# Kernel optimization log

Measured on AMD Instinct MI355X. Metric: run time of the kernel, lower is better.

## Reference

```python
import jax, jax.numpy as jnp
import numpy as np

B, NA, C, NG = 32, 32768, 81, 24
POS_IOU, NEG_IOU, NPR = 0.5, 0.4, 3
VXY, VWH = 0.1, 0.2
NEG_BIG = 1e30


def cxcywh_to_xyxy(b):
    xy, wh = b[..., :2], b[..., 2:]
    return jnp.concatenate([xy - 0.5 * wh, xy + 0.5 * wh], axis=-1)


def box_iou_xyxy(a, g):
    # a: [Na,4], g: [Ng,4] -> [Na,Ng]
    lt = jnp.maximum(a[:, None, :2], g[None, :, :2])
    rb = jnp.minimum(a[:, None, 2:], g[None, :, 2:])
    wh = jnp.clip(rb - lt, 0.0)
    inter = wh[..., 0] * wh[..., 1]
    area_a = (a[:, 2] - a[:, 0]) * (a[:, 3] - a[:, 1])
    area_g = (g[:, 2] - g[:, 0]) * (g[:, 3] - g[:, 1])
    union = area_a[:, None] + area_g[None, :] - inter
    return inter / jnp.maximum(union, 1e-12)


def encode_ssd(gt, anc):
    # gt, anc: [N,4] cxcywh
    txy = (gt[:, :2] - anc[:, :2]) / anc[:, 2:] / VXY
    twh = jnp.log(gt[:, 2:] / anc[:, 2:]) / VWH
    return jnp.concatenate([txy, twh], axis=-1)


def match_one(anchors, gt_b, gt_l):
    # anchors: [Na,4], gt_b: [Ng,4], gt_l: [Ng]
    iou = box_iou_xyxy(cxcywh_to_xyxy(anchors), cxcywh_to_xyxy(gt_b))  # [Na,Ng]
    iou_max = iou.max(axis=1)
    gt_idx = jnp.argmax(iou, axis=1)          # [Na]
    best_anchor = jnp.argmax(iou, axis=0)     # [Ng]
    pos = (iou_max >= POS_IOU).at[best_anchor].set(True)
    ign = (iou_max > NEG_IOU) & ~pos
    cls_t = jnp.where(pos, gt_l[gt_idx].astype(jnp.int32), jnp.where(ign, -1, 0))
    box_t = encode_ssd(gt_b[gt_idx], anchors) * pos[:, None].astype(jnp.float32)
    return cls_t, box_t, pos


def setup_inputs() -> dict:
    key = jax.random.key(0)
    k1, k2, k3, k4, k5, k6, k7 = jax.random.split(key, 7)
    cls_pred = jax.random.normal(k1, (B, NA, C), jnp.float32)
    box_pred = jax.random.normal(k2, (B, NA, 4), jnp.float32) * 0.5
    a_xy = jax.random.uniform(k3, (NA, 2), jnp.float32)
    a_wh = jax.random.uniform(k4, (NA, 2), jnp.float32, minval=0.02, maxval=0.5)
    anchors = jnp.concatenate([a_xy, a_wh], axis=-1)
    g_xy = jax.random.uniform(k5, (B, NG, 2), jnp.float32)
    g_wh = jax.random.uniform(k6, (B, NG, 2), jnp.float32, minval=0.05, maxval=0.4)
    gt_boxes = jnp.concatenate([g_xy, g_wh], axis=-1)
    gt_labels = jax.random.randint(k7, (B, NG), 1, C, jnp.int32)
    return {"cls_pred": cls_pred, "box_pred": box_pred, "anchors": anchors,
            "gt_boxes": gt_boxes, "gt_labels": gt_labels}


def reference(cls_pred, box_pred, anchors, gt_boxes, gt_labels):
    # matching is @torch.no_grad -> constants
    cls_t, box_t, pos = jax.vmap(lambda b, l: match_one(anchors, b, l))(gt_boxes, gt_labels)
    box_t = jax.lax.stop_gradient(box_t)

    logp = jax.nn.log_softmax(cls_pred, axis=-1)
    tgt = jnp.clip(cls_t, 0)
    ce = -jnp.take_along_axis(logp, tgt[..., None], axis=-1)[..., 0]  # [B,Na]

    posf = pos.astype(jnp.float32)
    num_pos = posf.sum(-1)                       # [B]
    pos_ce_sum = (ce * posf).sum(-1)
    neg_mask = cls_t == 0
    neg_count = neg_mask.sum(-1).astype(jnp.float32)

    # descending sort of negative CE (hard-negative mining)
    neg_sorted = -jnp.sort(-jnp.where(neg_mask, ce, -NEG_BIG), axis=-1)  # [B,Na]
    ranks = jnp.arange(NA, dtype=jnp.float32)[None, :]

    num_neg = jnp.minimum(NPR * num_pos, neg_count)
    topk_sum = (neg_sorted * (ranks < num_neg[:, None])).sum(-1)
    cls_pos = jnp.where(num_neg > 0,
                        (pos_ce_sum + topk_sum) / jnp.maximum(num_pos + num_neg, 1.0),
                        pos_ce_sum / jnp.maximum(num_pos, 1.0))

    num_neg0 = jnp.minimum(100.0, neg_count)
    topk0_sum = (neg_sorted * (ranks < num_neg0[:, None])).sum(-1)
    cls_zero = jnp.where(num_neg0 > 0, topk0_sum / jnp.maximum(num_neg0, 1.0), 0.0)

    cls_loss = jnp.where(num_pos > 0, cls_pos, cls_zero)

    d = box_pred - box_t
    ad = jnp.abs(d)
    sl1 = jnp.where(ad < 1.0, 0.5 * d * d, ad - 0.5)
    reg_sum = (sl1 * posf[..., None]).sum((-1, -2))
    reg = jnp.where(num_pos > 0, reg_sum / jnp.maximum(num_pos * 4.0, 1.0), 0.0)

    return cls_loss.mean(), reg.mean(), num_pos.sum() / B
```

## Files before the change

kernel.cpp:

```cpp
#include <hip/hip_runtime.h>
#include <math.h>

#define B_  32
#define NA_ 32768
#define C_  81
#define NG_ 24

__device__ inline float wave_sum_f(float v) {
  #pragma unroll
  for (int s = 32; s >= 1; s >>= 1) v += __shfl_xor(v, s);
  return v;
}
__device__ inline int wave_sum_i(int v) {
  #pragma unroll
  for (int s = 32; s >= 1; s >>= 1) v += __shfl_xor(v, s);
  return v;
}
__device__ inline unsigned long long shflx_u64(unsigned long long v, int s) {
  int lo = __shfl_xor((int)(unsigned)(v & 0xFFFFFFFFULL), s);
  int hi = __shfl_xor((int)(unsigned)(v >> 32), s);
  return ((unsigned long long)(unsigned)hi << 32) | (unsigned)lo;
}

__global__ __launch_bounds__(256) void k_match_b(
    const float* __restrict__ anchors, const float* __restrict__ gt_boxes,
    int* __restrict__ best_anchor,
    int* num_pos_g, int* notneg_g, float* pos_ce_g, float* reg_sum_g, float* out)
{
  const int g = blockIdx.x, b = blockIdx.y;
  const int tid = threadIdx.x, wave = tid >> 6, lane = tid & 63;
  if (g == 0 && b == 0) {
    if (tid < B_) { num_pos_g[tid] = 0; notneg_g[tid] = 0; pos_ce_g[tid] = 0.f; reg_sum_g[tid] = 0.f; }
    else if (tid < B_ + 3) out[tid - B_] = 0.f;
  }
  const float* gp = gt_boxes + ((size_t)b * NG_ + g) * 4;
  const float gx0 = gp[0] - 0.5f * gp[2], gy0 = gp[1] - 0.5f * gp[3];
  const float gx1 = gp[0] + 0.5f * gp[2], gy1 = gp[1] + 0.5f * gp[3];
  const float area_g = (gx1 - gx0) * (gy1 - gy0);
  unsigned long long key = 0ULL;
  #pragma unroll 4
  for (int i = 0; i < NA_ / 256; ++i) {
    const int a = i * 256 + tid;
    const float4 anc = ((const float4*)anchors)[a];
    const float ax0 = anc.x - 0.5f * anc.z, ay0 = anc.y - 0.5f * anc.w;
    const float ax1 = anc.x + 0.5f * anc.z, ay1 = anc.y + 0.5f * anc.w;
    float lx = fmaxf(ax0, gx0), ly = fmaxf(ay0, gy0);
    float rx = fminf(ax1, gx1), ry = fminf(ay1, gy1);
    float ww = fmaxf(rx - lx, 0.f), hh = fmaxf(ry - ly, 0.f);
    float inter = ww * hh;
    float uni = (ax1 - ax0) * (ay1 - ay0) + area_g - inter;
    float iou = inter / fmaxf(uni, 1e-12f);
    unsigned long long k2 =
        ((unsigned long long)__float_as_uint(iou) << 32) | (unsigned)(~(unsigned)a);
    if (k2 > key) key = k2;
  }
  #pragma unroll
  for (int s = 32; s >= 1; s >>= 1) {
    unsigned long long o = shflx_u64(key, s);
    if (o > key) key = o;
  }
  __shared__ unsigned long long red[4];
  if (lane == 0) red[wave] = key;
  __syncthreads();
  if (tid == 0) {
    unsigned long long k = red[0];
    for (int w = 1; w < 4; ++w) if (red[w] > k) k = red[w];
    best_anchor[b * NG_ + g] = (int)(~(unsigned)k);
  }
}

#define RPT  8
#define TPB2 256
__global__ __launch_bounds__(256, 2) void k_ce(
    const float* __restrict__ cls_pred, const float* __restrict__ box_pred,
    const float* __restrict__ anchors, const float* __restrict__ gt_boxes,
    const int* __restrict__ gt_labels, const int* __restrict__ best_anchor,
    int* __restrict__ neg_bits,
    int* __restrict__ num_pos_g, int* __restrict__ notneg_g,
    float* __restrict__ pos_ce_g, float* __restrict__ reg_sum_g)
{
  __shared__ float4 gt_xyxy[NG_];
  __shared__ float4 gt_cc[NG_];
  __shared__ float  gt_area[NG_];
  __shared__ int    label_sh[NG_];
  __shared__ int    best_a_sh[NG_];
  const int b = blockIdx.y;
  const int tid = threadIdx.x;
  const int wave = tid >> 6, lane = tid & 63;

  if (tid < NG_) {
    const float* g = gt_boxes + ((size_t)b * NG_ + tid) * 4;
    const float cx = g[0], cy = g[1], w = g[2], h = g[3];
    const float x0 = cx - 0.5f * w, y0 = cy - 0.5f * h;
    const float x1 = cx + 0.5f * w, y1 = cy + 0.5f * h;
    gt_xyxy[tid] = make_float4(x0, y0, x1, y1);
    gt_cc[tid]   = make_float4(cx, cy, w, h);
    gt_area[tid] = (x1 - x0) * (y1 - y0);
    label_sh[tid]  = gt_labels[b * NG_ + tid];
    best_a_sh[tid] = best_anchor[b * NG_ + tid];
  }
  __syncthreads();

  const int p = lane & 3;
  const int base = blockIdx.x * (TPB2 * RPT) + wave * (64 * RPT);

  int   npc = 0, nnc = 0;
  float pce = 0.f, regs = 0.f;

  #pragma unroll 1
  for (int it = 0; it < RPT; ++it) {
    const int a = base + it * 64 + lane;
    const size_t idx = (size_t)b * NA_ + a;

    const float4 anc = ((const float4*)anchors)[a];
    const float ax0 = anc.x - 0.5f * anc.z, ay0 = anc.y - 0.5f * anc.w;
    const float ax1 = anc.x + 0.5f * anc.z, ay1 = anc.y + 0.5f * anc.w;
    const float area_a = (ax1 - ax0) * (ay1 - ay0);
    float best_iou = -1.0f; int gi = 0;
    #pragma unroll 4
    for (int g = 0; g < NG_; ++g) {
      const float4 G = gt_xyxy[g];
      float lx = fmaxf(ax0, G.x), ly = fmaxf(ay0, G.y);
      float rx = fminf(ax1, G.z), ry = fminf(ay1, G.w);
      float ww = fmaxf(rx - lx, 0.f), hh = fmaxf(ry - ly, 0.f);
      float inter = ww * hh;
      float uni = area_a + gt_area[g] - inter;
      float iou = inter / fmaxf(uni, 1e-12f);
      if (iou > best_iou) { best_iou = iou; gi = g; }
    }
    bool pos = (best_iou >= 0.5f);
    #pragma unroll
    for (int g = 0; g < NG_; ++g) pos = pos || (best_a_sh[g] == a);
    const bool ign = (best_iou > 0.4f) && !pos;
    const bool neg = !pos && !ign;
    const int tgt = pos ? label_sh[gi] : 0;

    const size_t d0 = idx * 81;
    const float4* w4 = (const float4*)(cls_pred + (d0 & ~(size_t)3));
    float s0 = 0.f, s1 = 0.f, s2 = 0.f, s3 = 0.f;
    #pragma unroll
    for (int k = 0; k < 21; ++k) {
      float4 v = w4[k];
      if (k == 0) {
        v.x = (p > 0) ? -1e30f : v.x;
        v.y = (p > 1) ? -1e30f : v.y;
        v.z = (p > 2) ? -1e30f : v.z;
      }
      if (k == 20) {
        v.y = (p < 1) ? -1e30f : v.y;
        v.z = (p < 2) ? -1e30f : v.z;
        v.w = (p < 3) ? -1e30f : v.w;
      }
      s0 += __expf(v.x); s1 += __expf(v.y);
      s2 += __expf(v.z); s3 += __expf(v.w);
    }
    const float sum = (s0 + s1) + (s2 + s3);
    const float tv = cls_pred[d0 + tgt];
    const float ce = fmaxf(__logf(sum) - tv, 0.f);

    neg_bits[idx] = neg ? __float_as_int(ce) : -1;

    npc += pos;
    nnc += (pos || ign);
    if (pos) {
      pce += ce;
      const float4 bp = ((const float4*)box_pred)[idx];
      const float4 G  = gt_cc[gi];
      const float tx = (G.x - anc.x) / anc.z / 0.1f;
      const float ty = (G.y - anc.y) / anc.w / 0.1f;
      const float tw = logf(G.z / anc.z) / 0.2f;
      const float th = logf(G.w / anc.w) / 0.2f;
      float d, ad;
      d = bp.x - tx; ad = fabsf(d); regs += (ad < 1.f) ? 0.5f * d * d : (ad - 0.5f);
      d = bp.y - ty; ad = fabsf(d); regs += (ad < 1.f) ? 0.5f * d * d : (ad - 0.5f);
      d = bp.z - tw; ad = fabsf(d); regs += (ad < 1.f) ? 0.5f * d * d : (ad - 0.5f);
      d = bp.w - th; ad = fabsf(d); regs += (ad < 1.f) ? 0.5f * d * d : (ad - 0.5f);
    }
  }

  const int   np_w  = wave_sum_i(npc);
  const int   nn_w  = wave_sum_i(nnc);
  const float pce_w = wave_sum_f(pce);
  const float reg_w = wave_sum_f(regs);
  if (lane == 0) {
    if (np_w) atomicAdd(&num_pos_g[b], np_w);
    if (nn_w) atomicAdd(&notneg_g[b], nn_w);
    if (pce_w != 0.f) atomicAdd(&pos_ce_g[b], pce_w);
    if (reg_w != 0.f) atomicAdd(&reg_sum_g[b], reg_w);
  }
}

__global__ __launch_bounds__(1024) void k_select(
    const int* __restrict__ neg_bits,
    const int* __restrict__ num_pos_g, const int* __restrict__ notneg_g,
    const float* __restrict__ pos_ce_g, const float* __restrict__ reg_sum_g,
    float* __restrict__ out)
{
  const int b = blockIdx.x;
  const int t = threadIdx.x;
  const int wave = t >> 6, lane = t & 63;
  __shared__ unsigned cnt_sh[32];
  __shared__ float f1_sh[16], f0_sh[16];
  __shared__ unsigned cg_sh[16];
  if (t < 32) cnt_sh[t] = 0;
  int v[32];
  const int4* src4 = (const int4*)(neg_bits + (size_t)b * NA_);
  #pragma unroll
  for (int i = 0; i < 8; ++i) *(int4*)&v[4 * i] = src4[t + (i << 10)];
  const int np = num_pos_g[b];
  const int negc = NA_ - notneg_g[b];
  const int k1 = min(3 * np, negc);
  const int k0 = min(100, negc);
  __syncthreads();
  int T1 = 0, T0 = 0;
  for (int bit = 30; bit >= 0; --bit) {
    const int t1 = T1 | (1 << bit);
    const int t0 = T0 | (1 << bit);
    unsigned c = 0;
    #pragma unroll
    for (int i = 0; i < 32; ++i) {
      if (v[i] >= t1) c += (1u << 16);
      if (v[i] >= t0) c += 1u;
    }
    #pragma unroll
    for (int s = 32; s >= 1; s >>= 1) c += __shfl_xor(c, s);
    if (lane == 0) atomicAdd(&cnt_sh[bit], c);
    __syncthreads();
    const unsigned sum = cnt_sh[bit];
    if ((int)(sum >> 16) >= k1 && k1 > 0) T1 = t1;
    if ((int)(sum & 0xFFFFu) >= k0 && k0 > 0) T0 = t0;
  }
  float s1 = 0.f, s0 = 0.f; unsigned cg = 0;
  #pragma unroll
  for (int i = 0; i < 32; ++i) {
    const int x = v[i];
    if (x > T1) { s1 += __int_as_float(x); cg += (1u << 16); }
    if (x > T0) { s0 += __int_as_float(x); cg += 1u; }
  }
  #pragma unroll
  for (int s = 32; s >= 1; s >>= 1) {
    s1 += __shfl_xor(s1, s); s0 += __shfl_xor(s0, s); cg += __shfl_xor(cg, s);
  }
  if (lane == 0) { f1_sh[wave] = s1; f0_sh[wave] = s0; cg_sh[wave] = cg; }
  __syncthreads();
  if (t == 0) {
    float S1 = 0.f, S0 = 0.f; unsigned CG = 0;
    for (int w = 0; w < 16; ++w) { S1 += f1_sh[w]; S0 += f0_sh[w]; CG += cg_sh[w]; }
    const int cg1 = (int)(CG >> 16), cg0 = (int)(CG & 0xFFFFu);
    const float topk1 = (k1 > 0) ? (S1 + (float)(k1 - cg1) * __int_as_float(T1)) : 0.f;
    const float topk0 = (k0 > 0) ? (S0 + (float)(k0 - cg0) * __int_as_float(T0)) : 0.f;
    const float npf = (float)np;
    const float pce = pos_ce_g[b];
    float cls;
    if (np > 0)
      cls = (k1 > 0) ? (pce + topk1) / fmaxf(npf + (float)k1, 1.f)
                     : pce / fmaxf(npf, 1.f);
    else
      cls = (k0 > 0) ? topk0 / fmaxf((float)k0, 1.f) : 0.f;
    const float reg = (np > 0) ? reg_sum_g[b] / fmaxf(npf * 4.f, 1.f) : 0.f;
    atomicAdd(&out[0], cls * (1.0f / B_));
    atomicAdd(&out[1], reg * (1.0f / B_));
    atomicAdd(&out[2], npf * (1.0f / B_));
  }
}

extern "C" void kernel_launch(void* const* d_in, const int* in_sizes, int n_in,
                              void* d_out, int out_size, void* d_ws, size_t ws_size,
                              hipStream_t stream) {
  const float* cls_pred  = (const float*)d_in[0];
  const float* box_pred  = (const float*)d_in[1];
  const float* anchors   = (const float*)d_in[2];
  const float* gt_boxes  = (const float*)d_in[3];
  const int*   gt_labels = (const int*)d_in[4];
  float* out = (float*)d_out;

  char* ws = (char*)d_ws;
  int*   best_anchor = (int*)ws;
  int*   num_pos_g = (int*)(ws + 6144);
  int*   notneg_g  = (int*)(ws + 6144 + 128);
  float* pos_ce_g  = (float*)(ws + 6144 + 256);
  float* reg_sum_g = (float*)(ws + 6144 + 384);
  int*   neg_bits  = (int*)(ws + 8192);

  hipLaunchKernelGGL(k_match_b, dim3(NG_, B_), dim3(256), 0, stream,
                     anchors, gt_boxes, best_anchor,
                     num_pos_g, notneg_g, pos_ce_g, reg_sum_g, out);
  hipLaunchKernelGGL(k_ce, dim3(NA_ / (TPB2 * RPT), B_), dim3(TPB2), 0, stream,
                     cls_pred, box_pred, anchors, gt_boxes, gt_labels,
                     best_anchor, neg_bits,
                     num_pos_g, notneg_g, pos_ce_g, reg_sum_g);
  hipLaunchKernelGGL(k_select, dim3(B_), dim3(1024), 0, stream,
                     neg_bits, num_pos_g, notneg_g, pos_ce_g, reg_sum_g, out);
}
```

Baseline: 609.4 us.

## Stage cls_pred tiles into LDS via double-buffered global_load_lds in persistent k_ce

k_ce is restructured into single-wave blocks on a fixed 24x32 grid. Each block walks 64-anchor tiles with a grid stride and copies each tile's class logits into a double-buffered LDS area using coalesced global_load_lds DMA. The next tile is prefetched while the current one is processed, replacing the per-lane strided float4 reads of 324-byte rows straight from global memory. The cost is about 41 KB of LDS per block, which caps resident waves per CU, plus strided LDS reads that may cause bank conflicts.

```diff
diff --git a/kernel.cpp b/kernel.cpp
--- a/kernel.cpp
+++ b/kernel.cpp
@@ -5,6 +5,9 @@
 #define NA_ 32768
 #define C_  81
 #define NG_ 24
+
+typedef const __attribute__((address_space(1))) unsigned int* gas_ptr;
+typedef __attribute__((address_space(3))) unsigned int* las_ptr;
 
 __device__ inline float wave_sum_f(float v) {
   #pragma unroll
@@ -69,9 +72,23 @@
   }
 }
 
-#define RPT  8
-#define TPB2 256
-__global__ __launch_bounds__(256, 2) void k_ce(
+#define NBLK 24
+__device__ inline void stage_tile(const float* __restrict__ cls_pred,
+                                  int b, int tile, las_ptr lbase, int tid)
+{
+  const unsigned int* gtile =
+      (const unsigned int*)(cls_pred + ((size_t)b * NA_ + (size_t)tile * 64) * C_);
+  #pragma unroll
+  for (int k = 0; k < 20; ++k) {
+    const int chunk = k * 64 + tid;
+    __builtin_amdgcn_global_load_lds((gas_ptr)(gtile + (size_t)chunk * 4),
+                                     lbase + (size_t)(k * 64) * 4, 16, 0, 0);
+  }
+  __builtin_amdgcn_global_load_lds((gas_ptr)(gtile + 5120 + tid),
+                                   lbase + 5120, 4, 0, 0);
+}
+
+__global__ __launch_bounds__(64) void k_ce(
     const float* __restrict__ cls_pred, const float* __restrict__ box_pred,
     const float* __restrict__ anchors, const float* __restrict__ gt_boxes,
     const int* __restrict__ gt_labels, const int* __restrict__ best_anchor,
@@ -79,37 +96,47 @@
     int* __restrict__ num_pos_g, int* __restrict__ notneg_g,
     float* __restrict__ pos_ce_g, float* __restrict__ reg_sum_g)
 {
+  __shared__ float tile_sh[2][64 * C_];
   __shared__ float4 gt_xyxy[NG_];
   __shared__ float4 gt_cc[NG_];
   __shared__ float  gt_area[NG_];
   __shared__ int    label_sh[NG_];
   __shared__ int    best_a_sh[NG_];
   const int b = blockIdx.y;
-  const int tid = threadIdx.x;
-  const int wave = tid >> 6, lane = tid & 63;
-
-  if (tid < NG_) {
-    const float* g = gt_boxes + ((size_t)b * NG_ + tid) * 4;
+  const int j = blockIdx.x;
+  const int lane = threadIdx.x;
+
+  if (lane < NG_) {
+    const float* g = gt_boxes + ((size_t)b * NG_ + lane) * 4;
     const float cx = g[0], cy = g[1], w = g[2], h = g[3];
     const float x0 = cx - 0.5f * w, y0 = cy - 0.5f * h;
     const float x1 = cx + 0.5f * w, y1 = cy + 0.5f * h;
-    gt_xyxy[tid] = make_float4(x0, y0, x1, y1);
-    gt_cc[tid]   = make_float4(cx, cy, w, h);
-    gt_area[tid] = (x1 - x0) * (y1 - y0);
-    label_sh[tid]  = gt_labels[b * NG_ + tid];
-    best_a_sh[tid] = best_anchor[b * NG_ + tid];
+    gt_xyxy[lane] = make_float4(x0, y0, x1, y1);
+    gt_cc[lane]   = make_float4(cx, cy, w, h);
+    gt_area[lane] = (x1 - x0) * (y1 - y0);
+    label_sh[lane]  = gt_labels[b * NG_ + lane];
+    best_a_sh[lane] = best_anchor[b * NG_ + lane];
   }
   __syncthreads();
 
   const int p = lane & 3;
-  const int base = blockIdx.x * (TPB2 * RPT) + wave * (64 * RPT);
+  const int wbase = (81 * lane) & ~3;
 
   int   npc = 0, nnc = 0;
   float pce = 0.f, regs = 0.f;
 
-  #pragma unroll 1
-  for (int it = 0; it < RPT; ++it) {
-    const int a = base + it * 64 + lane;
+  int tj = j;
+  stage_tile(cls_pred, b, tj, (las_ptr)tile_sh[0], lane);
+  asm volatile("s_waitcnt vmcnt(0)" ::: "memory");
+  __builtin_amdgcn_sched_barrier(0);
+  int cur = 0;
+
+  while (true) {
+    const int tn = tj + NBLK;
+    const bool more = (tn < NA_ / 64);
+    if (more) stage_tile(cls_pred, b, tn, (las_ptr)tile_sh[cur ^ 1], lane);
+
+    const int a = tj * 64 + lane;
     const size_t idx = (size_t)b * NA_ + a;
 
     const float4 anc = ((const float4*)anchors)[a];
@@ -135,8 +162,7 @@
     const bool neg = !pos && !ign;
     const int tgt = pos ? label_sh[gi] : 0;
 
-    const size_t d0 = idx * 81;
-    const float4* w4 = (const float4*)(cls_pred + (d0 & ~(size_t)3));
+    const float4* w4 = (const float4*)&tile_sh[cur][wbase];
     float s0 = 0.f, s1 = 0.f, s2 = 0.f, s3 = 0.f;
     #pragma unroll
     for (int k = 0; k < 21; ++k) {
@@ -155,7 +181,7 @@
       s2 += __expf(v.z); s3 += __expf(v.w);
     }
     const float sum = (s0 + s1) + (s2 + s3);
-    const float tv = cls_pred[d0 + tgt];
+    const float tv = tile_sh[cur][81 * lane + tgt];
     const float ce = fmaxf(__logf(sum) - tv, 0.f);
 
     neg_bits[idx] = neg ? __float_as_int(ce) : -1;
@@ -176,6 +202,11 @@
       d = bp.z - tw; ad = fabsf(d); regs += (ad < 1.f) ? 0.5f * d * d : (ad - 0.5f);
       d = bp.w - th; ad = fabsf(d); regs += (ad < 1.f) ? 0.5f * d * d : (ad - 0.5f);
     }
+
+    if (!more) break;
+    asm volatile("s_waitcnt vmcnt(0)" ::: "memory");
+    __builtin_amdgcn_sched_barrier(0);
+    tj = tn; cur ^= 1;
   }
 
   const int   np_w  = wave_sum_i(npc);
@@ -285,7 +316,7 @@
   hipLaunchKernelGGL(k_match_b, dim3(NG_, B_), dim3(256), 0, stream,
                      anchors, gt_boxes, best_anchor,
                      num_pos_g, notneg_g, pos_ce_g, reg_sum_g, out);
-  hipLaunchKernelGGL(k_ce, dim3(NA_ / (TPB2 * RPT), B_), dim3(TPB2), 0, stream,
+  hipLaunchKernelGGL(k_ce, dim3(NBLK, B_), dim3(64), 0, stream,
                      cls_pred, box_pred, anchors, gt_boxes, gt_labels,
                      best_anchor, neg_bits,
                      num_pos_g, notneg_g, pos_ce_g, reg_sum_g);
```

Measured after the change: 562.9 us. 1.08x faster.
